# Optimization experiments

Hardware: AMD Instinct MI355X
Metric: run time of the kernel (lower is better)

## Reference

```python
import jax, jax.numpy as jnp
import numpy as np

M, N, K, C, H = 100000, 8192, 32, 256, 8
DH = C // H
FF = 512
R = (15, 15, 7)  # 2*MAXRANGE-1 per axis for MAXRANGE=[8,8,4]


def _layer_norm(x, g, b, eps=1e-5):
    mu = jnp.mean(x, axis=-1, keepdims=True)
    xc = x - mu
    var = jnp.mean(xc * xc, axis=-1, keepdims=True)
    return xc * jax.lax.rsqrt(var + eps) * g + b


def setup_inputs() -> dict:
    key = jax.random.key(0)
    ks = iter(jax.random.split(key, 40))
    d = {}
    d['voxel_features'] = jax.random.normal(next(ks), (M, C), jnp.float32)
    d['query_coords'] = jax.random.normal(next(ks), (N, 3), jnp.float32)
    d['query_indices'] = jax.random.randint(next(ks), (N,), 0, M)
    d['gather_indices'] = jax.random.randint(next(ks), (N, K), 0, M)
    d['gather_mask'] = jax.random.randint(next(ks), (N, K), 0, 2).astype(bool)
    d['rel_x'] = jax.random.randint(next(ks), (N, K), 0, R[0])
    d['rel_y'] = jax.random.randint(next(ks), (N, K), 0, R[1])
    d['rel_z'] = jax.random.randint(next(ks), (N, K), 0, R[2])
    s = 0.02
    # pos_proj: Conv1d(3, C, 1) == linear on coords
    d['w_pos'] = jax.random.normal(next(ks), (3, C), jnp.float32) * s
    d['b_pos'] = jnp.zeros((C,), jnp.float32)
    for nm in ['q', 'k', 'v', 'proj']:
        d['w_' + nm] = jax.random.normal(next(ks), (C, C), jnp.float32) * (C ** -0.5)
        d['b_' + nm] = jnp.zeros((C,), jnp.float32)
    d['ln1_g'] = jnp.ones((C,), jnp.float32); d['ln1_b'] = jnp.zeros((C,), jnp.float32)
    d['ln2_g'] = jnp.ones((C,), jnp.float32); d['ln2_b'] = jnp.zeros((C,), jnp.float32)
    d['w_ff1'] = jax.random.normal(next(ks), (C, FF), jnp.float32) * (C ** -0.5)
    d['b_ff1'] = jnp.zeros((FF,), jnp.float32)
    d['w_ff2'] = jax.random.normal(next(ks), (FF, C), jnp.float32) * (FF ** -0.5)
    d['b_ff2'] = jnp.zeros((C,), jnp.float32)
    # per-axis relative position tables: [H, DH, 2W-1] for q-side and k-side
    for m in ['q', 'k']:
        for ax, r in zip(['x', 'y', 'z'], R):
            d[f'pos_{m}{ax}'] = jax.random.normal(next(ks), (H, DH, r), jnp.float32) * s
    return d


def reference(voxel_features, query_coords, query_indices, gather_indices, gather_mask,
              rel_x, rel_y, rel_z,
              w_pos, b_pos, w_q, b_q, w_k, b_k, w_v, b_v, w_proj, b_proj,
              ln1_g, ln1_b, ln2_g, ln2_b, w_ff1, b_ff1, w_ff2, b_ff2,
              pos_qx, pos_qy, pos_qz, pos_kx, pos_ky, pos_kz):
    x = _layer_norm(voxel_features, ln1_g, ln1_b)           # [M, C] pre-norm
    # gather window centers (queries) + positional projection of coords
    q_in = x[query_indices] + jax.nn.relu(query_coords @ w_pos + b_pos)  # [N, C]
    kv_in = x[gather_indices]                                # [N, K, C]
    kv_in = jnp.where(gather_mask[..., None], 0.0, kv_in)
    q = (q_in @ w_q + b_q).reshape(N, H, DH)
    k = (kv_in @ w_k + b_k).reshape(N, K, H, DH)
    v = (kv_in @ w_v + b_v).reshape(N, K, H, DH)
    logits = jnp.einsum('nhd,nkhd->nhk', q, k) * (DH ** -0.5)  # [N, H, K]
    # query-side per-axis relative position bias: contract q with table, gather at rel idx
    for pos, rel in ((pos_qx, rel_x), (pos_qy, rel_y), (pos_qz, rel_z)):
        qp = jnp.einsum('nhd,hdr->nhr', q, pos)              # [N, H, R]
        logits = logits + jnp.take_along_axis(qp, rel[:, None, :], axis=2)
    # key-side per-axis relative position bias
    for pos, rel in ((pos_kx, rel_x), (pos_ky, rel_y), (pos_kz, rel_z)):
        kp = jnp.einsum('nkhd,hdr->nkhr', k, pos)            # [N, K, H, R]
        bias = jnp.take_along_axis(kp, rel[:, :, None, None], axis=3)[..., 0]  # [N, K, H]
        logits = logits + bias.transpose(0, 2, 1)
    logits = jnp.where(gather_mask[:, None, :], -1e9, logits)
    attn = jax.nn.softmax(logits, axis=-1)
    out = jnp.einsum('nhk,nkhd->nhd', attn, v).reshape(N, C) @ w_proj + b_proj
    act = voxel_features[query_indices] + out                # residual (pre-norm block)
    h = jax.nn.relu(_layer_norm(act, ln2_g, ln2_b) @ w_ff1 + b_ff1) @ w_ff2 + b_ff2
    return act + h                                           # [N, C]
```

## Files before the change

### kernel.cpp

```cpp
#include <hip/hip_runtime.h>
#include <hip/hip_bf16.h>
#include <math.h>

#define MV   100000
#define NQ   8192
#define KN   32
#define CH   256
#define NH   8
#define DHD  32
#define FFD  512
#define NG   (NQ*KN)
#define QPW  37
#define QPN  (NH*QPW)
#define QPL  320
#define ASTR 40

typedef __bf16 bf16x8 __attribute__((ext_vector_type(8)));
typedef float  f32x4  __attribute__((ext_vector_type(4)));

__device__ __forceinline__ float bf2f(unsigned short u) {
    return __uint_as_float(((unsigned int)u) << 16);
}
__device__ __forceinline__ unsigned short f2bf(float f) {
    unsigned int x = __float_as_uint(f);
    unsigned int r = x + 0x7FFFu + ((x >> 16) & 1u);
    return (unsigned short)(r >> 16);
}
__device__ __forceinline__ void glds16(const unsigned short* g, unsigned short* l) {
    __builtin_amdgcn_global_load_lds(
        (const __attribute__((address_space(1))) void*)g,
        (__attribute__((address_space(3))) void*)l, 16, 0, 0);
}

__global__ __launch_bounds__(256) void k_detect_mask(const unsigned char* __restrict__ raw,
                                                     int* __restrict__ flags) {
    __shared__ int any;
    if (threadIdx.x == 0) any = 0;
    __syncthreads();
    const uint4* p = (const uint4*)raw;
    int i = blockIdx.x * 256 + threadIdx.x;
    uint4 v = p[i];
    if ((v.x | v.y | v.z | v.w) & 0xFFFFFF00u) any = 1;
    __syncthreads();
    if (threadIdx.x == 0) flags[blockIdx.x] = any;
}

__global__ __launch_bounds__(256) void k_prep(const float* __restrict__ w_k,
                                              const float* __restrict__ w_v,
                                              const float* __restrict__ w_ff1,
                                              const float* __restrict__ w_ff2,
                                              const float* __restrict__ w_proj,
                                              const float* __restrict__ w_q,
                                              const float* __restrict__ b_k,
                                              const float* __restrict__ b_v,
                                              const float* __restrict__ pos_qx,
                                              const float* __restrict__ pos_qy,
                                              const float* __restrict__ pos_qz,
                                              const void* __restrict__ mask_raw,
                                              const int* __restrict__ flags,
                                              unsigned short* __restrict__ w_kv_t,
                                              unsigned short* __restrict__ w1_t,
                                              unsigned short* __restrict__ w2_t,
                                              unsigned short* __restrict__ wp_t,
                                              unsigned short* __restrict__ wq_t,
                                              unsigned short* __restrict__ wqp_t,
                                              float* __restrict__ bkv,
                                              float* __restrict__ zbias,
                                              int* __restrict__ mask_i) {
    __shared__ int bl;
    if (threadIdx.x == 0) {
        int a = 0;
        #pragma unroll 8
        for (int i = 0; i < 64; i++) a |= flags[i];
        bl = a;
    }
    __syncthreads();
    int byteLayout = bl;
    int idx = blockIdx.x * 256 + threadIdx.x;
    if (blockIdx.x == 0 && threadIdx.x < 512)
        bkv[threadIdx.x] = (threadIdx.x < 256) ? b_k[threadIdx.x]
                                               : b_v[threadIdx.x - 256];
    if (idx < QPL) zbias[idx] = 0.f;
    if (idx < NG) {
        int mv = byteLayout ? (int)((const unsigned char*)mask_raw)[idx]
                            : ((const int*)mask_raw)[idx];
        mask_i[idx] = (mv != 0) ? 1 : 0;
    }
    if (idx < 512 * 256) {
        int col = idx >> 8, j = idx & 255;
        float v = (col < 256) ? w_k[j * 256 + col] : w_v[j * 256 + (col - 256)];
        w_kv_t[idx] = f2bf(v);
    }
    if (idx < 512 * 256) {
        int n = idx >> 8, k = idx & 255;
        w1_t[idx] = f2bf(w_ff1[k * FFD + n]);
    }
    if (idx < 256 * 512) {
        int n = idx >> 9, k = idx & 511;
        w2_t[idx] = f2bf(w_ff2[k * CH + n]);
    }
    if (idx < 256 * 256) {
        int n = idx >> 8, k = idx & 255;
        wp_t[idx] = f2bf(w_proj[k * CH + n]);
        wq_t[idx] = f2bf(w_q[k * CH + n]);
    }
    if (idx < QPL * 256) {
        int col = idx >> 8, k = idx & 255;
        float v = 0.f;
        if (col < QPN) {
            int h = col / QPW, r = col % QPW;
            int h2 = k >> 5, d = k & 31;
            if (h2 == h) {
                if (r < 15)      v = pos_qx[(h * DHD + d) * 15 + r];
                else if (r < 30) v = pos_qy[(h * DHD + d) * 15 + (r - 15)];
                else             v = pos_qz[(h * DHD + d) * 7  + (r - 30)];
            }
        }
        wqp_t[idx] = f2bf(v);
    }
}

__global__ __launch_bounds__(256) void k_posc(const float* __restrict__ pos_kx,
                                              const float* __restrict__ pos_ky,
                                              const float* __restrict__ pos_kz,
                                              float* __restrict__ comb) {
    int idx = blockIdx.x * 256 + threadIdx.x;
    if (idx >= 8 * 15 * 15 * 7 * 32) return;
    int d = idx & 31, r = idx >> 5;
    int rz = r % 7;  r /= 7;
    int ry = r % 15; r /= 15;
    int rx = r % 15; int h = r / 15;
    comb[idx] = pos_kx[(h * DHD + d) * 15 + rx]
              + pos_ky[(h * DHD + d) * 15 + ry]
              + pos_kz[(h * DHD + d) * 7  + rz];
}

__global__ __launch_bounds__(256) void k_ln(const float* __restrict__ x,
                                            const float* __restrict__ g,
                                            const float* __restrict__ b,
                                            unsigned short* __restrict__ o,
                                            int nrows) {
    int wid = threadIdx.x >> 6, lane = threadIdx.x & 63;
    int row = blockIdx.x * 4 + wid;
    if (row >= nrows) return;
    const float4 v = *(const float4*)(x + (size_t)row * CH + lane * 4);
    float s  = v.x + v.y + v.z + v.w;
    float sq = v.x * v.x + v.y * v.y + v.z * v.z + v.w * v.w;
    #pragma unroll
    for (int off = 1; off < 64; off <<= 1) {
        s  += __shfl_xor(s,  off);
        sq += __shfl_xor(sq, off);
    }
    float mu  = s * (1.f / CH);
    float var = sq * (1.f / CH) - mu * mu;
    float rs  = rsqrtf(var + 1e-5f);
    float4 gv = *(const float4*)(g + lane * 4);
    float4 bv = *(const float4*)(b + lane * 4);
    ushort4 ov;
    ov.x = f2bf((v.x - mu) * rs * gv.x + bv.x);
    ov.y = f2bf((v.y - mu) * rs * gv.y + bv.y);
    ov.z = f2bf((v.z - mu) * rs * gv.z + bv.z);
    ov.w = f2bf((v.w - mu) * rs * gv.w + bv.w);
    *(ushort4*)(o + (size_t)row * CH + lane * 4) = ov;
}

__global__ __launch_bounds__(256) void k_qin(const unsigned short* __restrict__ ln_x,
                                             const float* __restrict__ coords,
                                             const int* __restrict__ qidx,
                                             const float* __restrict__ w_pos,
                                             const float* __restrict__ b_pos,
                                             unsigned short* __restrict__ qin) {
    int c = threadIdx.x;
    int nb = blockIdx.x * 8;
    float wp0 = w_pos[c], wp1 = w_pos[CH + c], wp2 = w_pos[2 * CH + c], bp = b_pos[c];
    #pragma unroll
    for (int qq = 0; qq < 8; qq++) {
        int n = nb + qq;
        float p = bp + coords[n * 3] * wp0 + coords[n * 3 + 1] * wp1 + coords[n * 3 + 2] * wp2;
        p = fmaxf(p, 0.f);
        int qi = qidx[n];
        qin[(size_t)n * CH + c] = f2bf(bf2f(ln_x[(size_t)qi * CH + c]) + p);
    }
}

__global__ __launch_bounds__(256) void k_kv(const unsigned short* __restrict__ ln_x,
                                            const unsigned short* __restrict__ w_kv_t,
                                            const float* __restrict__ bkv,
                                            unsigned short* __restrict__ kv) {
    __shared__ __align__(16) unsigned short As[128 * 32];
    __shared__ __align__(16) unsigned short Bs[128 * 32];
    const int tid = threadIdx.x;
    const int w = tid >> 6, l = tid & 63;
    const int wr = w >> 1, wc = w & 1;
    const int rowbase = blockIdx.y * 128;
    const int col0 = blockIdx.x * 128;
    const int sr = l >> 2, sq = l & 3;
    int ra0 = rowbase + w * 16 + sr;      if (ra0 >= MV) ra0 = MV - 1;
    int ra1 = rowbase + 64 + w * 16 + sr; if (ra1 >= MV) ra1 = MV - 1;
    const unsigned short* pa0 = ln_x + (size_t)ra0 * CH + sq * 8;
    const unsigned short* pa1 = ln_x + (size_t)ra1 * CH + sq * 8;
    const unsigned short* pb0 = w_kv_t + (size_t)(col0 + w * 16 + sr) * CH + sq * 8;
    const unsigned short* pb1 = w_kv_t + (size_t)(col0 + 64 + w * 16 + sr) * CH + sq * 8;
    unsigned short* lA0 = As + w * 512;
    unsigned short* lA1 = As + 2048 + w * 512;
    unsigned short* lB0 = Bs + w * 512;
    unsigned short* lB1 = Bs + 2048 + w * 512;

    f32x4 acc[4][4];
    #pragma unroll
    for (int mt = 0; mt < 4; mt++)
        #pragma unroll
        for (int nt = 0; nt < 4; nt++)
            acc[mt][nt] = (f32x4){0.f, 0.f, 0.f, 0.f};

    const int ml = l & 15, qd = l >> 4;
    for (int kk = 0; kk < CH; kk += 32) {
        __syncthreads();
        glds16(pa0 + kk, lA0);
        glds16(pa1 + kk, lA1);
        glds16(pb0 + kk, lB0);
        glds16(pb1 + kk, lB1);
        __syncthreads();
        bf16x8 af[4], bf[4];
        #pragma unroll
        for (int mt = 0; mt < 4; mt++)
            af[mt] = *(const bf16x8*)(As + (wr * 64 + mt * 16 + ml) * 32 + qd * 8);
        #pragma unroll
        for (int nt = 0; nt < 4; nt++)
            bf[nt] = *(const bf16x8*)(Bs + (wc * 64 + nt * 16 + ml) * 32 + qd * 8);
        #pragma unroll
        for (int mt = 0; mt < 4; mt++)
            #pragma unroll
            for (int nt = 0; nt < 4; nt++)
                acc[mt][nt] = __builtin_amdgcn_mfma_f32_16x16x32_bf16(af[mt], bf[nt], acc[mt][nt], 0, 0, 0);
    }

    float bb[4];
    #pragma unroll
    for (int nt = 0; nt < 4; nt++)
        bb[nt] = bkv[col0 + wc * 64 + nt * 16 + ml];
    unsigned short* trs = As;
    #pragma unroll
    for (int mt = 0; mt < 4; mt++) {
        __syncthreads();
        #pragma unroll
        for (int nt = 0; nt < 4; nt++) {
            int lcol = wc * 64 + nt * 16 + ml;
            #pragma unroll
            for (int i = 0; i < 4; i++)
                trs[wr * 2048 + (qd * 4 + i) * 128 + lcol] = f2bf(acc[mt][nt][i] + bb[nt]);
        }
        __syncthreads();
        int rl = tid >> 4, cc = (tid & 15) * 8;
        int g0 = rowbase + mt * 16 + rl;
        int g1 = rowbase + 64 + mt * 16 + rl;
        if (g0 < MV)
            *(uint4*)(kv + (size_t)g0 * 512 + col0 + cc) = *(const uint4*)(trs + rl * 128 + cc);
        if (g1 < MV)
            *(uint4*)(kv + (size_t)g1 * 512 + col0 + cc) = *(const uint4*)(trs + 2048 + rl * 128 + cc);
    }
}

template <int KD, int EPI, int LDO>
__global__ __launch_bounds__(256) void k_mm(const unsigned short* __restrict__ A,
                                            const unsigned short* __restrict__ Bt_g,
                                            const float* __restrict__ bias,
                                            const float* __restrict__ res,
                                            const int* __restrict__ qidx,
                                            unsigned short* __restrict__ out_bf,
                                            float* __restrict__ out_f) {
    __shared__ __align__(16) unsigned short As[128 * ASTR];
    __shared__ __align__(16) unsigned short Bs[64 * ASTR];
    int tid = threadIdx.x;
    int w = tid >> 6, l = tid & 63;
    int rowbase = blockIdx.y * 128;
    int col0 = blockIdx.x * 64;
    int r0 = tid >> 2, qt = tid & 3;
    const unsigned short* a0p = A + (size_t)(rowbase + r0) * KD + qt * 8;
    const unsigned short* a1p = A + (size_t)(rowbase + 64 + r0) * KD + qt * 8;

    f32x4 acc[2][4];
    #pragma unroll
    for (int mt = 0; mt < 2; mt++)
        #pragma unroll
        for (int nt = 0; nt < 4; nt++)
            acc[mt][nt] = (f32x4){0.f, 0.f, 0.f, 0.f};

    const int ml = l & 15, qd = l >> 4;
    for (int kk = 0; kk < KD; kk += 32) {
        __syncthreads();
        uint4 v0 = *(const uint4*)(a0p + kk);
        uint4 v1 = *(const uint4*)(a1p + kk);
        *(uint4*)(As + r0 * ASTR + qt * 8)        = v0;
        *(uint4*)(As + (64 + r0) * ASTR + qt * 8) = v1;
        {
            uint4 bv = *(const uint4*)(Bt_g + (size_t)(col0 + r0) * KD + kk + qt * 8);
            *(uint4*)(Bs + r0 * ASTR + qt * 8) = bv;
        }
        __syncthreads();
        bf16x8 a0 = *(const bf16x8*)(As + (w * 32 + ml) * ASTR + qd * 8);
        bf16x8 a1 = *(const bf16x8*)(As + (w * 32 + 16 + ml) * ASTR + qd * 8);
        #pragma unroll
        for (int nt = 0; nt < 4; nt++) {
            bf16x8 bb = *(const bf16x8*)(Bs + (nt * 16 + ml) * ASTR + qd * 8);
            acc[0][nt] = __builtin_amdgcn_mfma_f32_16x16x32_bf16(a0, bb, acc[0][nt], 0, 0, 0);
            acc[1][nt] = __builtin_amdgcn_mfma_f32_16x16x32_bf16(a1, bb, acc[1][nt], 0, 0, 0);
        }
    }

    #pragma unroll
    for (int nt = 0; nt < 4; nt++) {
        int col = col0 + nt * 16 + ml;
        float bv = bias[col];
        #pragma unroll
        for (int mt = 0; mt < 2; mt++) {
            int rl = w * 32 + mt * 16 + qd * 4;
            #pragma unroll
            for (int i = 0; i < 4; i++) {
                int row = rowbase + rl + i;
                float v = acc[mt][nt][i] + bv;
                if (EPI == 0) {
                    out_bf[(size_t)row * LDO + col] = f2bf(fmaxf(v, 0.f));
                } else if (EPI == 1) {
                    out_f[(size_t)row * CH + col] = v + res[(size_t)row * CH + col];
                } else if (EPI == 2) {
                    int qi = qidx[row];
                    out_f[(size_t)row * CH + col] = v + res[(size_t)qi * CH + col];
                } else if (EPI == 3) {
                    out_f[(size_t)row * CH + col] = v;
                    out_bf[(size_t)row * CH + col] = f2bf(v);
                } else {
                    out_f[(size_t)row * LDO + col] = v;
                }
            }
        }
    }
}

__global__ __launch_bounds__(256) void k_attn(const float* __restrict__ qbuf,
                                              const float* __restrict__ qp,
                                              const unsigned short* __restrict__ kvmat,
                                              const int* __restrict__ gidx,
                                              const int* __restrict__ mask_i,
                                              const int* __restrict__ rel_x,
                                              const int* __restrict__ rel_y,
                                              const int* __restrict__ rel_z,
                                              const float* __restrict__ comb,
                                              float* __restrict__ attn) {
    __shared__ float q_s[1024];
    __shared__ float qp_s[4 * QPL];
    int tid = threadIdx.x;
    int qb = blockIdx.x * 4;
    for (int i = tid; i < 1024; i += 256) q_s[i] = qbuf[(size_t)qb * CH + i];
    for (int i = tid; i < 4 * QPL; i += 256) qp_s[i] = qp[(size_t)qb * QPL + i];
    __syncthreads();
    int h = tid >> 5, k = tid & 31;
    const float scale = 0.17677669529663687f;
    for (int qq = 0; qq < 4; qq++) {
        int n = qb + qq;
        int gi = n * KN + k;
        int mk = mask_i[gi];
        float lg = -1e9f;
        if (!mk) {
            int rx = rel_x[gi], ry = rel_y[gi], rz = rel_z[gi];
            int g = gidx[gi];
            const uint4* kp = (const uint4*)(kvmat + (size_t)g * 512 + h * DHD);
            float kv[32];
            #pragma unroll
            for (int j = 0; j < 4; j++) {
                uint4 u = kp[j];
                kv[j * 8 + 0] = bf2f((unsigned short)(u.x & 0xFFFF));
                kv[j * 8 + 1] = bf2f((unsigned short)(u.x >> 16));
                kv[j * 8 + 2] = bf2f((unsigned short)(u.y & 0xFFFF));
                kv[j * 8 + 3] = bf2f((unsigned short)(u.y >> 16));
                kv[j * 8 + 4] = bf2f((unsigned short)(u.z & 0xFFFF));
                kv[j * 8 + 5] = bf2f((unsigned short)(u.z >> 16));
                kv[j * 8 + 6] = bf2f((unsigned short)(u.w & 0xFFFF));
                kv[j * 8 + 7] = bf2f((unsigned short)(u.w >> 16));
            }
            const float* cp = comb + ((((h * 15 + rx) * 15 + ry) * 7 + rz) << 5);
            float s1 = 0.f, s2 = 0.f;
            const float* qrow = q_s + qq * CH + h * DHD;
            #pragma unroll
            for (int d = 0; d < 32; d++) {
                s1 += kv[d] * qrow[d];
                s2 += kv[d] * cp[d];
            }
            lg = s1 * scale + s2
               + qp_s[qq * QPL + h * QPW + rx]
               + qp_s[qq * QPL + h * QPW + 15 + ry]
               + qp_s[qq * QPL + h * QPW + 30 + rz];
        }
        float mx = lg;
        #pragma unroll
        for (int off = 1; off <= 16; off <<= 1) mx = fmaxf(mx, __shfl_xor(mx, off));
        float e = mk ? 0.f : __expf(lg - mx);
        float sm = e;
        #pragma unroll
        for (int off = 1; off <= 16; off <<= 1) sm += __shfl_xor(sm, off);
        attn[(size_t)n * 256 + tid] = (sm > 0.f) ? e / sm : 0.f;
    }
}

__global__ __launch_bounds__(256) void k_av(const unsigned short* __restrict__ kvmat,
                                            const int* __restrict__ gidx,
                                            const int* __restrict__ mask_i,
                                            const float* __restrict__ attn,
                                            const float* __restrict__ b_v,
                                            unsigned short* __restrict__ attnln) {
    __shared__ float attn_s[4 * 256];
    __shared__ int mask_s[4 * 32];
    int tid = threadIdx.x;
    int w = tid >> 6, l = tid & 63;
    int qb = blockIdx.x * 4;
    for (int i = tid; i < 1024; i += 256) attn_s[i] = attn[(size_t)qb * 256 + i];
    if (tid < 128) mask_s[tid] = mask_i[qb * 32 + tid];
    __syncthreads();
    int n = qb + w;
    int h = l >> 3;
    float a0 = 0.f, a1 = 0.f, a2 = 0.f, a3 = 0.f;
    int nm = 0;
    for (int k = 0; k < KN; k++) {
        if (mask_s[w * 32 + k]) continue;
        nm++;
        int g = gidx[n * 32 + k];
        ushort4 v4 = *(const ushort4*)(kvmat + (size_t)g * 512 + 256 + l * 4);
        float av = attn_s[w * 256 + h * 32 + k];
        a0 += av * bf2f(v4.x);
        a1 += av * bf2f(v4.y);
        a2 += av * bf2f(v4.z);
        a3 += av * bf2f(v4.w);
    }
    int col = l * 4;
    if (nm == 0) {
        a0 = b_v[col]; a1 = b_v[col + 1]; a2 = b_v[col + 2]; a3 = b_v[col + 3];
    }
    ushort4 o;
    o.x = f2bf(a0); o.y = f2bf(a1); o.z = f2bf(a2); o.w = f2bf(a3);
    *(ushort4*)(attnln + (size_t)n * CH + col) = o;
}

extern "C" void kernel_launch(void* const* d_in, const int* in_sizes, int n_in,
                              void* d_out, int out_size, void* d_ws, size_t ws_size,
                              hipStream_t stream) {
    (void)in_sizes; (void)n_in; (void)out_size; (void)ws_size;
    const float* vox    = (const float*)d_in[0];
    const float* coords = (const float*)d_in[1];
    const int*   qidx   = (const int*)d_in[2];
    const int*   gidx   = (const int*)d_in[3];
    const void*  mraw   = d_in[4];
    const int*   rel_x  = (const int*)d_in[5];
    const int*   rel_y  = (const int*)d_in[6];
    const int*   rel_z  = (const int*)d_in[7];
    const float* w_pos  = (const float*)d_in[8];
    const float* b_pos  = (const float*)d_in[9];
    const float* w_q    = (const float*)d_in[10];
    const float* b_q    = (const float*)d_in[11];
    const float* w_k    = (const float*)d_in[12];
    const float* b_k    = (const float*)d_in[13];
    const float* w_v    = (const float*)d_in[14];
    const float* b_v    = (const float*)d_in[15];
    const float* w_proj = (const float*)d_in[16];
    const float* b_proj = (const float*)d_in[17];
    const float* ln1_g  = (const float*)d_in[18];
    const float* ln1_b  = (const float*)d_in[19];
    const float* ln2_g  = (const float*)d_in[20];
    const float* ln2_b  = (const float*)d_in[21];
    const float* w_ff1  = (const float*)d_in[22];
    const float* b_ff1  = (const float*)d_in[23];
    const float* w_ff2  = (const float*)d_in[24];
    const float* b_ff2  = (const float*)d_in[25];
    const float* pos_qx = (const float*)d_in[26];
    const float* pos_qy = (const float*)d_in[27];
    const float* pos_qz = (const float*)d_in[28];
    const float* pos_kx = (const float*)d_in[29];
    const float* pos_ky = (const float*)d_in[30];
    const float* pos_kz = (const float*)d_in[31];

    char* p = (char*)d_ws;
    auto take = [&](size_t n) { char* r = p; p += (n + 255) & ~(size_t)255; return r; };
    unsigned short* ln_x    = (unsigned short*)take((size_t)MV * CH * 2);
    unsigned short* w_kv_t  = (unsigned short*)take((size_t)512 * 256 * 2);
    unsigned short* w1_t    = (unsigned short*)take((size_t)512 * 256 * 2);
    unsigned short* w2_t    = (unsigned short*)take((size_t)256 * 512 * 2);
    unsigned short* wp_t    = (unsigned short*)take((size_t)256 * 256 * 2);
    unsigned short* wq_t    = (unsigned short*)take((size_t)256 * 256 * 2);
    unsigned short* wqp_t   = (unsigned short*)take((size_t)QPL * 256 * 2);
    float*          bkv     = (float*)take(512 * 4);
    float*          zbias   = (float*)take(QPL * 4);
    int*            flags   = (int*)take(64 * 4);
    int*            mask_i  = (int*)take((size_t)NG * 4);
    float*          comb    = (float*)take((size_t)8 * 15 * 15 * 7 * 32 * 4);
    unsigned short* qin     = (unsigned short*)take((size_t)NQ * CH * 2);
    float*          qbuf    = (float*)take((size_t)NQ * CH * 4);
    unsigned short* qbf     = (unsigned short*)take((size_t)NQ * CH * 2);
    float*          qp      = (float*)take((size_t)NQ * QPL * 4);
    unsigned short* kvmat   = (unsigned short*)take((size_t)MV * 512 * 2);
    float*          attn    = (float*)take((size_t)NQ * 256 * 4);
    unsigned short* attnln  = (unsigned short*)take((size_t)NQ * CH * 2);
    float*          actbuf  = (float*)take((size_t)NQ * CH * 4);
    unsigned short* actln   = (unsigned short*)take((size_t)NQ * CH * 2);
    unsigned short* hbuf    = (unsigned short*)take((size_t)NQ * FFD * 2);

    hipLaunchKernelGGL(k_detect_mask, dim3(64), dim3(256), 0, stream,
                       (const unsigned char*)mraw, flags);
    hipLaunchKernelGGL(k_prep, dim3(NG / 256), dim3(256), 0, stream,
                       w_k, w_v, w_ff1, w_ff2, w_proj, w_q, b_k, b_v,
                       pos_qx, pos_qy, pos_qz, mraw, flags,
                       w_kv_t, w1_t, w2_t, wp_t, wq_t, wqp_t, bkv, zbias, mask_i);
    hipLaunchKernelGGL(k_posc, dim3((8 * 15 * 15 * 7 * 32 + 255) / 256), dim3(256), 0, stream,
                       pos_kx, pos_ky, pos_kz, comb);
    hipLaunchKernelGGL(k_ln, dim3(MV / 4 + 1), dim3(256), 0, stream,
                       vox, ln1_g, ln1_b, ln_x, MV);
    hipLaunchKernelGGL(k_qin, dim3(NQ / 8), dim3(256), 0, stream,
                       ln_x, coords, qidx, w_pos, b_pos, qin);
    hipLaunchKernelGGL(k_kv, dim3(4, (MV + 127) / 128), dim3(256), 0, stream,
                       ln_x, w_kv_t, bkv, kvmat);
    hipLaunchKernelGGL(HIP_KERNEL_NAME(k_mm<256, 3, CH>), dim3(4, NQ / 128), dim3(256), 0, stream,
                       qin, wq_t, b_q, (const float*)nullptr, (const int*)nullptr,
                       qbf, qbuf);
    hipLaunchKernelGGL(HIP_KERNEL_NAME(k_mm<256, 4, QPL>), dim3(QPL / 64, NQ / 128), dim3(256), 0, stream,
                       qbf, wqp_t, zbias, (const float*)nullptr, (const int*)nullptr,
                       (unsigned short*)nullptr, qp);
    hipLaunchKernelGGL(k_attn, dim3(NQ / 4), dim3(256), 0, stream,
                       qbuf, qp, kvmat, gidx, mask_i, rel_x, rel_y, rel_z, comb, attn);
    hipLaunchKernelGGL(k_av, dim3(NQ / 4), dim3(256), 0, stream,
                       kvmat, gidx, mask_i, attn, b_v, attnln);
    hipLaunchKernelGGL(HIP_KERNEL_NAME(k_mm<256, 2, CH>), dim3(4, NQ / 128), dim3(256), 0, stream,
                       attnln, wp_t, b_proj, vox, qidx,
                       (unsigned short*)nullptr, actbuf);
    hipLaunchKernelGGL(k_ln, dim3(NQ / 4), dim3(256), 0, stream,
                       actbuf, ln2_g, ln2_b, actln, NQ);
    hipLaunchKernelGGL(HIP_KERNEL_NAME(k_mm<256, 0, FFD>), dim3(8, NQ / 128), dim3(256), 0, stream,
                       actln, w1_t, b_ff1, (const float*)nullptr, (const int*)nullptr,
                       hbuf, (float*)nullptr);
    hipLaunchKernelGGL(HIP_KERNEL_NAME(k_mm<512, 1, CH>), dim3(4, NQ / 128), dim3(256), 0, stream,
                       hbuf, w2_t, b_ff2, actbuf, (const int*)nullptr,
                       (unsigned short*)nullptr, (float*)d_out);
}
```

Baseline: 406.3 us.

## Skip K/V projection for unreferenced voxels and fuse attention with AV

Marks voxels referenced by an unmasked gather in a touched bitmap during prep, then has the K/V projection kernel write only touched rows. The kernel now keeps the full A row-tile in LDS and loops over all four column tiles, so the activations are loaded once per block instead of once per column tile. The softmax and attention-times-V kernels are fused so probabilities stay in shared memory instead of going through a global buffer. This adds a memset and scattered byte writes in prep, and the larger LDS footprint (64KB+) lowers occupancy. Skipped rows still run MFMA but are not stored.

```diff
diff --git a/kernel.cpp b/kernel.cpp
--- a/kernel.cpp
+++ b/kernel.cpp
@@ -57,6 +57,7 @@
                                               const float* __restrict__ pos_qy,
                                               const float* __restrict__ pos_qz,
                                               const void* __restrict__ mask_raw,
+                                              const int* __restrict__ gidx,
                                               const int* __restrict__ flags,
                                               unsigned short* __restrict__ w_kv_t,
                                               unsigned short* __restrict__ w1_t,
@@ -66,7 +67,8 @@
                                               unsigned short* __restrict__ wqp_t,
                                               float* __restrict__ bkv,
                                               float* __restrict__ zbias,
-                                              int* __restrict__ mask_i) {
+                                              int* __restrict__ mask_i,
+                                              unsigned char* __restrict__ touched) {
     __shared__ int bl;
     if (threadIdx.x == 0) {
         int a = 0;
@@ -85,6 +87,7 @@
         int mv = byteLayout ? (int)((const unsigned char*)mask_raw)[idx]
                             : ((const int*)mask_raw)[idx];
         mask_i[idx] = (mv != 0) ? 1 : 0;
+        if (mv == 0) touched[gidx[idx]] = 1;
     }
     if (idx < 512 * 256) {
         int col = idx >> 8, j = idx & 255;
@@ -186,78 +189,88 @@
 __global__ __launch_bounds__(256) void k_kv(const unsigned short* __restrict__ ln_x,
                                             const unsigned short* __restrict__ w_kv_t,
                                             const float* __restrict__ bkv,
+                                            const unsigned char* __restrict__ touched,
                                             unsigned short* __restrict__ kv) {
-    __shared__ __align__(16) unsigned short As[128 * 32];
-    __shared__ __align__(16) unsigned short Bs[128 * 32];
+    __shared__ __align__(16) unsigned short As[8 * 4096];
+    __shared__ __align__(16) unsigned short Bs[4096];
     const int tid = threadIdx.x;
     const int w = tid >> 6, l = tid & 63;
     const int wr = w >> 1, wc = w & 1;
-    const int rowbase = blockIdx.y * 128;
-    const int col0 = blockIdx.x * 128;
+    const int rowbase = blockIdx.x * 128;
     const int sr = l >> 2, sq = l & 3;
-    int ra0 = rowbase + w * 16 + sr;      if (ra0 >= MV) ra0 = MV - 1;
-    int ra1 = rowbase + 64 + w * 16 + sr; if (ra1 >= MV) ra1 = MV - 1;
-    const unsigned short* pa0 = ln_x + (size_t)ra0 * CH + sq * 8;
-    const unsigned short* pa1 = ln_x + (size_t)ra1 * CH + sq * 8;
-    const unsigned short* pb0 = w_kv_t + (size_t)(col0 + w * 16 + sr) * CH + sq * 8;
-    const unsigned short* pb1 = w_kv_t + (size_t)(col0 + 64 + w * 16 + sr) * CH + sq * 8;
+    const int ml = l & 15, qd = l >> 4;
+
+    int ra0 = rowbase + w * 16 + sr;
+    int ra1 = rowbase + 64 + w * 16 + sr;
+    int ok0 = (ra0 < MV) && touched[ra0 < MV ? ra0 : 0];
+    int ok1 = (ra1 < MV) && touched[ra1 < MV ? ra1 : 0];
+    const unsigned short* pa0 = ln_x + (size_t)(ok0 ? ra0 : rowbase) * CH + sq * 8;
+    const unsigned short* pa1 = ln_x + (size_t)(ok1 ? ra1 : rowbase) * CH + sq * 8;
     unsigned short* lA0 = As + w * 512;
     unsigned short* lA1 = As + 2048 + w * 512;
     unsigned short* lB0 = Bs + w * 512;
     unsigned short* lB1 = Bs + 2048 + w * 512;
 
-    f32x4 acc[4][4];
     #pragma unroll
-    for (int mt = 0; mt < 4; mt++)
+    for (int c = 0; c < 8; c++) {
+        glds16(pa0 + c * 32, lA0 + c * 4096);
+        glds16(pa1 + c * 32, lA1 + c * 4096);
+    }
+
+    for (int ct = 0; ct < 4; ct++) {
+        const int col0 = ct * 128;
+        const unsigned short* pb0 = w_kv_t + (size_t)(col0 + w * 16 + sr) * CH + sq * 8;
+        const unsigned short* pb1 = w_kv_t + (size_t)(col0 + 64 + w * 16 + sr) * CH + sq * 8;
+        f32x4 acc[4][4];
+        #pragma unroll
+        for (int mt = 0; mt < 4; mt++)
+            #pragma unroll
+            for (int nt = 0; nt < 4; nt++)
+                acc[mt][nt] = (f32x4){0.f, 0.f, 0.f, 0.f};
+
+        for (int c = 0; c < 8; c++) {
+            __syncthreads();
+            glds16(pb0 + c * 32, lB0);
+            glds16(pb1 + c * 32, lB1);
+            __syncthreads();
+            bf16x8 af[4], bf[4];
+            const unsigned short* Ac = As + c * 4096;
+            #pragma unroll
+            for (int mt = 0; mt < 4; mt++)
+                af[mt] = *(const bf16x8*)(Ac + (wr * 64 + mt * 16 + ml) * 32 + qd * 8);
+            #pragma unroll
+            for (int nt = 0; nt < 4; nt++)
+                bf[nt] = *(const bf16x8*)(Bs + (wc * 64 + nt * 16 + ml) * 32 + qd * 8);
+            #pragma unroll
+            for (int mt = 0; mt < 4; mt++)
+                #pragma unroll
+                for (int nt = 0; nt < 4; nt++)
+                    acc[mt][nt] = __builtin_amdgcn_mfma_f32_16x16x32_bf16(af[mt], bf[nt], acc[mt][nt], 0, 0, 0);
+        }
+
+        float bb[4];
         #pragma unroll
         for (int nt = 0; nt < 4; nt++)
-            acc[mt][nt] = (f32x4){0.f, 0.f, 0.f, 0.f};
-
-    const int ml = l & 15, qd = l >> 4;
-    for (int kk = 0; kk < CH; kk += 32) {
-        __syncthreads();
-        glds16(pa0 + kk, lA0);
-        glds16(pa1 + kk, lA1);
-        glds16(pb0 + kk, lB0);
-        glds16(pb1 + kk, lB1);
-        __syncthreads();
-        bf16x8 af[4], bf[4];
-        #pragma unroll
-        for (int mt = 0; mt < 4; mt++)
-            af[mt] = *(const bf16x8*)(As + (wr * 64 + mt * 16 + ml) * 32 + qd * 8);
-        #pragma unroll
-        for (int nt = 0; nt < 4; nt++)
-            bf[nt] = *(const bf16x8*)(Bs + (wc * 64 + nt * 16 + ml) * 32 + qd * 8);
-        #pragma unroll
-        for (int mt = 0; mt < 4; mt++)
-            #pragma unroll
-            for (int nt = 0; nt < 4; nt++)
-                acc[mt][nt] = __builtin_amdgcn_mfma_f32_16x16x32_bf16(af[mt], bf[nt], acc[mt][nt], 0, 0, 0);
-    }
-
-    float bb[4];
-    #pragma unroll
-    for (int nt = 0; nt < 4; nt++)
-        bb[nt] = bkv[col0 + wc * 64 + nt * 16 + ml];
-    unsigned short* trs = As;
-    #pragma unroll
-    for (int mt = 0; mt < 4; mt++) {
-        __syncthreads();
-        #pragma unroll
-        for (int nt = 0; nt < 4; nt++) {
-            int lcol = wc * 64 + nt * 16 + ml;
-            #pragma unroll
-            for (int i = 0; i < 4; i++)
-                trs[wr * 2048 + (qd * 4 + i) * 128 + lcol] = f2bf(acc[mt][nt][i] + bb[nt]);
-        }
-        __syncthreads();
-        int rl = tid >> 4, cc = (tid & 15) * 8;
-        int g0 = rowbase + mt * 16 + rl;
-        int g1 = rowbase + 64 + mt * 16 + rl;
-        if (g0 < MV)
-            *(uint4*)(kv + (size_t)g0 * 512 + col0 + cc) = *(const uint4*)(trs + rl * 128 + cc);
-        if (g1 < MV)
-            *(uint4*)(kv + (size_t)g1 * 512 + col0 + cc) = *(const uint4*)(trs + 2048 + rl * 128 + cc);
+            bb[nt] = bkv[col0 + wc * 64 + nt * 16 + ml];
+        #pragma unroll
+        for (int mt = 0; mt < 4; mt++) {
+            __syncthreads();
+            #pragma unroll
+            for (int nt = 0; nt < 4; nt++) {
+                int lcol = wc * 64 + nt * 16 + ml;
+                #pragma unroll
+                for (int i = 0; i < 4; i++)
+                    Bs[wr * 2048 + (qd * 4 + i) * 128 + lcol] = f2bf(acc[mt][nt][i] + bb[nt]);
+            }
+            __syncthreads();
+            int rl = tid >> 4, cc = (tid & 15) * 8;
+            int g0 = rowbase + mt * 16 + rl;
+            int g1 = rowbase + 64 + mt * 16 + rl;
+            if (g0 < MV && touched[g0])
+                *(uint4*)(kv + (size_t)g0 * 512 + col0 + cc) = *(const uint4*)(Bs + rl * 128 + cc);
+            if (g1 < MV && touched[g1])
+                *(uint4*)(kv + (size_t)g1 * 512 + col0 + cc) = *(const uint4*)(Bs + 2048 + rl * 128 + cc);
+        }
     }
 }
 
@@ -337,29 +350,33 @@
     }
 }
 
-__global__ __launch_bounds__(256) void k_attn(const float* __restrict__ qbuf,
-                                              const float* __restrict__ qp,
-                                              const unsigned short* __restrict__ kvmat,
-                                              const int* __restrict__ gidx,
-                                              const int* __restrict__ mask_i,
-                                              const int* __restrict__ rel_x,
-                                              const int* __restrict__ rel_y,
-                                              const int* __restrict__ rel_z,
-                                              const float* __restrict__ comb,
-                                              float* __restrict__ attn) {
+__global__ __launch_bounds__(256) void k_attn2(const float* __restrict__ qbuf,
+                                               const float* __restrict__ qp,
+                                               const unsigned short* __restrict__ kvmat,
+                                               const int* __restrict__ gidx,
+                                               const int* __restrict__ mask_i,
+                                               const int* __restrict__ rel_x,
+                                               const int* __restrict__ rel_y,
+                                               const int* __restrict__ rel_z,
+                                               const float* __restrict__ comb,
+                                               const float* __restrict__ b_v,
+                                               unsigned short* __restrict__ attnln) {
     __shared__ float q_s[1024];
     __shared__ float qp_s[4 * QPL];
+    __shared__ float attn_s[4 * 256];
+    __shared__ int mask_s[4 * 32];
     int tid = threadIdx.x;
     int qb = blockIdx.x * 4;
     for (int i = tid; i < 1024; i += 256) q_s[i] = qbuf[(size_t)qb * CH + i];
     for (int i = tid; i < 4 * QPL; i += 256) qp_s[i] = qp[(size_t)qb * QPL + i];
+    if (tid < 128) mask_s[tid] = mask_i[qb * 32 + tid];
     __syncthreads();
     int h = tid >> 5, k = tid & 31;
     const float scale = 0.17677669529663687f;
     for (int qq = 0; qq < 4; qq++) {
         int n = qb + qq;
         int gi = n * KN + k;
-        int mk = mask_i[gi];
+        int mk = mask_s[qq * 32 + k];
         float lg = -1e9f;
         if (!mk) {
             int rx = rel_x[gi], ry = rel_y[gi], rz = rel_z[gi];
@@ -398,34 +415,21 @@
         float sm = e;
         #pragma unroll
         for (int off = 1; off <= 16; off <<= 1) sm += __shfl_xor(sm, off);
-        attn[(size_t)n * 256 + tid] = (sm > 0.f) ? e / sm : 0.f;
-    }
-}
-
-__global__ __launch_bounds__(256) void k_av(const unsigned short* __restrict__ kvmat,
-                                            const int* __restrict__ gidx,
-                                            const int* __restrict__ mask_i,
-                                            const float* __restrict__ attn,
-                                            const float* __restrict__ b_v,
-                                            unsigned short* __restrict__ attnln) {
-    __shared__ float attn_s[4 * 256];
-    __shared__ int mask_s[4 * 32];
-    int tid = threadIdx.x;
+        attn_s[qq * 256 + tid] = (sm > 0.f) ? e / sm : 0.f;
+    }
+    __syncthreads();
+
     int w = tid >> 6, l = tid & 63;
-    int qb = blockIdx.x * 4;
-    for (int i = tid; i < 1024; i += 256) attn_s[i] = attn[(size_t)qb * 256 + i];
-    if (tid < 128) mask_s[tid] = mask_i[qb * 32 + tid];
-    __syncthreads();
     int n = qb + w;
-    int h = l >> 3;
+    int hh = l >> 3;
     float a0 = 0.f, a1 = 0.f, a2 = 0.f, a3 = 0.f;
     int nm = 0;
-    for (int k = 0; k < KN; k++) {
-        if (mask_s[w * 32 + k]) continue;
+    for (int kk = 0; kk < KN; kk++) {
+        if (mask_s[w * 32 + kk]) continue;
         nm++;
-        int g = gidx[n * 32 + k];
+        int g = gidx[n * 32 + kk];
         ushort4 v4 = *(const ushort4*)(kvmat + (size_t)g * 512 + 256 + l * 4);
-        float av = attn_s[w * 256 + h * 32 + k];
+        float av = attn_s[w * 256 + hh * 32 + kk];
         a0 += av * bf2f(v4.x);
         a1 += av * bf2f(v4.y);
         a2 += av * bf2f(v4.z);
@@ -490,42 +494,43 @@
     float*          zbias   = (float*)take(QPL * 4);
     int*            flags   = (int*)take(64 * 4);
     int*            mask_i  = (int*)take((size_t)NG * 4);
+    unsigned char*  touched = (unsigned char*)take(MV);
     float*          comb    = (float*)take((size_t)8 * 15 * 15 * 7 * 32 * 4);
     unsigned short* qin     = (unsigned short*)take((size_t)NQ * CH * 2);
     float*          qbuf    = (float*)take((size_t)NQ * CH * 4);
     unsigned short* qbf     = (unsigned short*)take((size_t)NQ * CH * 2);
     float*          qp      = (float*)take((size_t)NQ * QPL * 4);
     unsigned short* kvmat   = (unsigned short*)take((size_t)MV * 512 * 2);
-    float*          attn    = (float*)take((size_t)NQ * 256 * 4);
     unsigned short* attnln  = (unsigned short*)take((size_t)NQ * CH * 2);
     float*          actbuf  = (float*)take((size_t)NQ * CH * 4);
     unsigned short* actln   = (unsigned short*)take((size_t)NQ * CH * 2);
     unsigned short* hbuf    = (unsigned short*)take((size_t)NQ * FFD * 2);
 
+    hipMemsetAsync(touched, 0, MV, stream);
     hipLaunchKernelGGL(k_detect_mask, dim3(64), dim3(256), 0, stream,
                        (const unsigned char*)mraw, flags);
     hipLaunchKernelGGL(k_prep, dim3(NG / 256), dim3(256), 0, stream,
                        w_k, w_v, w_ff1, w_ff2, w_proj, w_q, b_k, b_v,
-                       pos_qx, pos_qy, pos_qz, mraw, flags,
-                       w_kv_t, w1_t, w2_t, wp_t, wq_t, wqp_t, bkv, zbias, mask_i);
+                       pos_qx, pos_qy, pos_qz, mraw, gidx, flags,
+                       w_kv_t, w1_t, w2_t, wp_t, wq_t, wqp_t, bkv, zbias,
+                       mask_i, touched);
     hipLaunchKernelGGL(k_posc, dim3((8 * 15 * 15 * 7 * 32 + 255) / 256), dim3(256), 0, stream,
                        pos_kx, pos_ky, pos_kz, comb);
     hipLaunchKernelGGL(k_ln, dim3(MV / 4 + 1), dim3(256), 0, stream,
                        vox, ln1_g, ln1_b, ln_x, MV);
     hipLaunchKernelGGL(k_qin, dim3(NQ / 8), dim3(256), 0, stream,
                        ln_x, coords, qidx, w_pos, b_pos, qin);
-    hipLaunchKernelGGL(k_kv, dim3(4, (MV + 127) / 128), dim3(256), 0, stream,
-                       ln_x, w_kv_t, bkv, kvmat);
+    hipLaunchKernelGGL(k_kv, dim3((MV + 127) / 128), dim3(256), 0, stream,
+                       ln_x, w_kv_t, bkv, touched, kvmat);
     hipLaunchKernelGGL(HIP_KERNEL_NAME(k_mm<256, 3, CH>), dim3(4, NQ / 128), dim3(256), 0, stream,
                        qin, wq_t, b_q, (const float*)nullptr, (const int*)nullptr,
                        qbf, qbuf);
     hipLaunchKernelGGL(HIP_KERNEL_NAME(k_mm<256, 4, QPL>), dim3(QPL / 64, NQ / 128), dim3(256), 0, stream,
                        qbf, wqp_t, zbias, (const float*)nullptr, (const int*)nullptr,
                        (unsigned short*)nullptr, qp);
-    hipLaunchKernelGGL(k_attn, dim3(NQ / 4), dim3(256), 0, stream,
-                       qbuf, qp, kvmat, gidx, mask_i, rel_x, rel_y, rel_z, comb, attn);
-    hipLaunchKernelGGL(k_av, dim3(NQ / 4), dim3(256), 0, stream,
-                       kvmat, gidx, mask_i, attn, b_v, attnln);
+    hipLaunchKernelGGL(k_attn2, dim3(NQ / 4), dim3(256), 0, stream,
+                       qbuf, qp, kvmat, gidx, mask_i, rel_x, rel_y, rel_z,
+                       comb, b_v, attnln);
     hipLaunchKernelGGL(HIP_KERNEL_NAME(k_mm<256, 2, CH>), dim3(4, NQ / 128), dim3(256), 0, stream,
                        attnln, wp_t, b_proj, vox, qidx,
                        (unsigned short*)nullptr, actbuf);
```

New measurement: 416.8 us. 2.6% more time.
